# Optimization experiments

Measured on AMD Instinct MI355X. Metric: run time of the kernel, lower is better.

The kernel has to match this reference:

```python
import jax, jax.numpy as jnp
import numpy as np

EPS = 1e-05  # epsilon for Cholesky regularization


def setup_inputs() -> dict:
    key = jax.random.key(0)
    k1, k2, k3 = jax.random.split(key, 3)
    B, H, W, C, I = 32, 64, 64, 64, 4
    x = jax.random.normal(k1, (B, H, W, C, I), dtype=jnp.float32)
    # affine params: identity-like weight plus noise, small bias
    eye = jnp.eye(I, dtype=jnp.float32)[..., None]  # (I, I, 1)
    weight = jnp.broadcast_to(eye, (I, I, C)) + 0.05 * jax.random.normal(k2, (I, I, C), dtype=jnp.float32)
    bias = 0.05 * jax.random.normal(k3, (I, C), dtype=jnp.float32)
    return {"x": x, "weight": weight, "bias": bias}


def reference(x, weight, bias):
    # x: (B, H, W, C, I); training-mode batch stats
    B, H, W, C, I = x.shape
    n = B * H * W
    mean = jnp.mean(x, axis=(0, 1, 2))                       # (C, I)
    xc = x - mean                                            # centered, (B,H,W,C,I)
    cov = jnp.einsum('bhwci,bhwcj->cij', xc, xc) / n         # per-channel (I, I) covariance
    cov = cov + EPS * jnp.eye(I, dtype=x.dtype)
    L = jnp.linalg.cholesky(cov)                             # (C, I, I), lower
    eye = jnp.broadcast_to(jnp.eye(I, dtype=x.dtype), (C, I, I))
    Linv = jax.lax.linalg.triangular_solve(L, eye, left_side=True, lower=True)  # (C, I, I)
    x_norm = jnp.einsum('cij,bhwcj->bhwci', Linv, xc)        # whitened
    # affine: out_i = sum_j weight[i, j, c] * x_norm[..., c, j] + bias[i, c]
    out = jnp.einsum('ijc,bhwcj->bhwci', weight, x_norm) + bias.T
    return out
```

## Files before the change

### kernel.cpp

```cpp
#include <hip/hip_runtime.h>
#include <math.h>

#define EPSREG 1e-5f

typedef float vf4 __attribute__((ext_vector_type(4)));

__global__ __launch_bounds__(256) void stats_kernel(const vf4* __restrict__ x,
                                                    float* __restrict__ stats,
                                                    int pos_per_slice) {
    int tid  = threadIdx.x;
    int c    = tid & 63;
    int lane = tid >> 6;
    int s    = blockIdx.x * 4 + lane;

    const vf4* xp = x + (size_t)s * pos_per_slice * 64 + c;

    float a0=0.f,a1=0.f,a2=0.f,a3=0.f;
    float p00=0.f,p01=0.f,p02=0.f,p03=0.f;
    float p11=0.f,p12=0.f,p13=0.f;
    float p22=0.f,p23=0.f,p33=0.f;

    for (int it = 0; it < pos_per_slice; it += 8) {
        vf4 v[8];
        #pragma unroll
        for (int u = 0; u < 8; ++u) v[u] = xp[(it + u) * 64];
        #pragma unroll
        for (int u = 0; u < 8; ++u) {
            float x0 = v[u].x, x1 = v[u].y, x2 = v[u].z, x3 = v[u].w;
            a0 += x0; a1 += x1; a2 += x2; a3 += x3;
            p00 += x0*x0; p01 += x0*x1; p02 += x0*x2; p03 += x0*x3;
            p11 += x1*x1; p12 += x1*x2; p13 += x1*x3;
            p22 += x2*x2; p23 += x2*x3;
            p33 += x3*x3;
        }
    }

    __shared__ float sm[14 * 256];
    float vals[14] = {a0,a1,a2,a3,p00,p01,p02,p03,p11,p12,p13,p22,p23,p33};
    #pragma unroll
    for (int k = 0; k < 14; ++k) sm[k * 256 + tid] = vals[k];
    __syncthreads();

    if (tid < 64) {
        #pragma unroll
        for (int k = 0; k < 14; ++k) {
            float v = sm[k*256 + tid] + sm[k*256 + 64 + tid]
                    + sm[k*256 + 128 + tid] + sm[k*256 + 192 + tid];
            atomicAdd(&stats[k * 64 + tid], v);
        }
    }
}

__global__ void solve_kernel(const float* __restrict__ stats,
                             const float* __restrict__ weight,
                             const float* __restrict__ bias,
                             float* __restrict__ params,
                             float inv_n) {
    int c = threadIdx.x;
    if (c >= 64) return;

    float m0 = stats[0*64+c]*inv_n, m1 = stats[1*64+c]*inv_n;
    float m2 = stats[2*64+c]*inv_n, m3 = stats[3*64+c]*inv_n;
    float c00 = stats[4*64+c]*inv_n  - m0*m0 + EPSREG;
    float c01 = stats[5*64+c]*inv_n  - m0*m1;
    float c02 = stats[6*64+c]*inv_n  - m0*m2;
    float c03 = stats[7*64+c]*inv_n  - m0*m3;
    float c11 = stats[8*64+c]*inv_n  - m1*m1 + EPSREG;
    float c12 = stats[9*64+c]*inv_n  - m1*m2;
    float c13 = stats[10*64+c]*inv_n - m1*m3;
    float c22 = stats[11*64+c]*inv_n - m2*m2 + EPSREG;
    float c23 = stats[12*64+c]*inv_n - m2*m3;
    float c33 = stats[13*64+c]*inv_n - m3*m3 + EPSREG;

    float l00 = sqrtf(c00);
    float l10 = c01 / l00, l20 = c02 / l00, l30 = c03 / l00;
    float l11 = sqrtf(c11 - l10*l10);
    float l21 = (c12 - l20*l10) / l11;
    float l31 = (c13 - l30*l10) / l11;
    float l22 = sqrtf(c22 - l20*l20 - l21*l21);
    float l32 = (c23 - l30*l20 - l31*l21) / l22;
    float l33 = sqrtf(c33 - l30*l30 - l31*l31 - l32*l32);

    float i00 = 1.f / l00, i11 = 1.f / l11, i22 = 1.f / l22, i33 = 1.f / l33;
    float i10 = -i11 * (l10 * i00);
    float i20 = -i22 * (l20 * i00 + l21 * i10);
    float i21 = -i22 * (l21 * i11);
    float i30 = -i33 * (l30 * i00 + l31 * i10 + l32 * i20);
    float i31 = -i33 * (l31 * i11 + l32 * i21);
    float i32 = -i33 * (l32 * i22);

    float Li[4][4] = {{i00, 0.f, 0.f, 0.f},
                      {i10, i11, 0.f, 0.f},
                      {i20, i21, i22, 0.f},
                      {i30, i31, i32, i33}};

    float* pp = params + c * 25;
    #pragma unroll
    for (int i = 0; i < 4; ++i) {
        float w0 = weight[(i*4 + 0)*64 + c];
        float w1 = weight[(i*4 + 1)*64 + c];
        float w2 = weight[(i*4 + 2)*64 + c];
        float w3 = weight[(i*4 + 3)*64 + c];
        #pragma unroll
        for (int j = 0; j < 4; ++j) {
            pp[i*4 + j] = w0*Li[0][j] + w1*Li[1][j] + w2*Li[2][j] + w3*Li[3][j];
        }
    }
    pp[16] = m0; pp[17] = m1; pp[18] = m2; pp[19] = m3;
    pp[20] = bias[0*64 + c];
    pp[21] = bias[1*64 + c];
    pp[22] = bias[2*64 + c];
    pp[23] = bias[3*64 + c];
    pp[24] = 0.f;
}

__global__ __launch_bounds__(256) void apply_kernel(const vf4* __restrict__ x,
                                                    vf4* __restrict__ out,
                                                    const float* __restrict__ params,
                                                    int total4) {
    int tid0   = blockIdx.x * blockDim.x + threadIdx.x;
    int stride = gridDim.x * blockDim.x;
    int c      = tid0 & 63;

    const float* pp = params + c * 25;
    float M[16];
    #pragma unroll
    for (int k = 0; k < 16; ++k) M[k] = pp[k];
    float m0 = pp[16], m1 = pp[17], m2 = pp[18], m3 = pp[19];
    float b0 = pp[20], b1 = pp[21], b2 = pp[22], b3 = pp[23];

    int i = tid0;
    for (; i + 3 * stride < total4; i += 4 * stride) {
        vf4 v[4];
        #pragma unroll
        for (int u = 0; u < 4; ++u) v[u] = x[i + u * stride];
        #pragma unroll
        for (int u = 0; u < 4; ++u) {
            float x0 = v[u].x - m0, x1 = v[u].y - m1, x2 = v[u].z - m2, x3 = v[u].w - m3;
            vf4 o;
            o.x = M[0]*x0  + M[1]*x1  + M[2]*x2  + M[3]*x3  + b0;
            o.y = M[4]*x0  + M[5]*x1  + M[6]*x2  + M[7]*x3  + b1;
            o.z = M[8]*x0  + M[9]*x1  + M[10]*x2 + M[11]*x3 + b2;
            o.w = M[12]*x0 + M[13]*x1 + M[14]*x2 + M[15]*x3 + b3;
            __builtin_nontemporal_store(o, &out[i + u * stride]);
        }
    }
    for (; i < total4; i += stride) {
        vf4 v = x[i];
        float x0 = v.x - m0, x1 = v.y - m1, x2 = v.z - m2, x3 = v.w - m3;
        vf4 o;
        o.x = M[0]*x0  + M[1]*x1  + M[2]*x2  + M[3]*x3  + b0;
        o.y = M[4]*x0  + M[5]*x1  + M[6]*x2  + M[7]*x3  + b1;
        o.z = M[8]*x0  + M[9]*x1  + M[10]*x2 + M[11]*x3 + b2;
        o.w = M[12]*x0 + M[13]*x1 + M[14]*x2 + M[15]*x3 + b3;
        __builtin_nontemporal_store(o, &out[i]);
    }
}

extern "C" void kernel_launch(void* const* d_in, const int* in_sizes, int n_in,
                              void* d_out, int out_size, void* d_ws, size_t ws_size,
                              hipStream_t stream) {
    const float* x      = (const float*)d_in[0];
    const float* weight = (const float*)d_in[1];
    const float* bias   = (const float*)d_in[2];
    float* out = (float*)d_out;

    float* stats  = (float*)d_ws;
    float* params = (float*)((char*)d_ws + 4096);

    int n_elem = in_sizes[0];
    int npos   = n_elem / 256;
    int total4 = n_elem / 4;

    (void)hipMemsetAsync(stats, 0, 14 * 64 * sizeof(float), stream);

    int pos_per_slice = npos / 2048;
    stats_kernel<<<512, 256, 0, stream>>>((const vf4*)x, stats, pos_per_slice);
    solve_kernel<<<1, 64, 0, stream>>>(stats, weight, bias, params, 1.0f / (float)npos);
    apply_kernel<<<2048, 256, 0, stream>>>((const vf4*)x, (vf4*)out, params, total4);
}
```

Baseline: 265.2 us.

## Fuse stats, solve and apply into one persistent kernel with grid barrier

Merges the three kernels into one 512-block kernel. Each block accumulates partial moments, atomically adds them, then waits on a global counter barrier. After the barrier every thread recomputes its channel's Cholesky/whitening matrix in registers and re-reads its own slice of x to write the output. This removes two launches and the params round-trip, and can let the second read of x hit in cache (x is 64 MiB, so reuse depends on the last-level cache). It relies on all 512 blocks being co-resident, otherwise the spin barrier deadlocks, and every thread now repeats the small solve.

```diff
diff --git a/kernel.cpp b/kernel.cpp
--- a/kernel.cpp
+++ b/kernel.cpp
@@ -2,25 +2,31 @@
 #include <math.h>
 
 #define EPSREG 1e-5f
+#define NBLOCKS 512
 
 typedef float vf4 __attribute__((ext_vector_type(4)));
 
-__global__ __launch_bounds__(256) void stats_kernel(const vf4* __restrict__ x,
+__global__ __launch_bounds__(256) void fused_kernel(const vf4* __restrict__ x,
+                                                    const float* __restrict__ weight,
+                                                    const float* __restrict__ bias,
+                                                    vf4* __restrict__ out,
                                                     float* __restrict__ stats,
-                                                    int pos_per_slice) {
+                                                    unsigned int* __restrict__ counter,
+                                                    int pps,
+                                                    float inv_n) {
     int tid  = threadIdx.x;
     int c    = tid & 63;
     int lane = tid >> 6;
     int s    = blockIdx.x * 4 + lane;
 
-    const vf4* xp = x + (size_t)s * pos_per_slice * 64 + c;
+    const vf4* xp = x + (size_t)s * pps * 64 + c;
 
     float a0=0.f,a1=0.f,a2=0.f,a3=0.f;
     float p00=0.f,p01=0.f,p02=0.f,p03=0.f;
     float p11=0.f,p12=0.f,p13=0.f;
     float p22=0.f,p23=0.f,p33=0.f;
 
-    for (int it = 0; it < pos_per_slice; it += 8) {
+    for (int it = 0; it < pps; it += 8) {
         vf4 v[8];
         #pragma unroll
         for (int u = 0; u < 8; ++u) v[u] = xp[(it + u) * 64];
@@ -36,9 +42,11 @@
     }
 
     __shared__ float sm[14 * 256];
-    float vals[14] = {a0,a1,a2,a3,p00,p01,p02,p03,p11,p12,p13,p22,p23,p33};
-    #pragma unroll
-    for (int k = 0; k < 14; ++k) sm[k * 256 + tid] = vals[k];
+    {
+        float vals[14] = {a0,a1,a2,a3,p00,p01,p02,p03,p11,p12,p13,p22,p23,p33};
+        #pragma unroll
+        for (int k = 0; k < 14; ++k) sm[k * 256 + tid] = vals[k];
+    }
     __syncthreads();
 
     if (tid < 64) {
@@ -49,28 +57,34 @@
             atomicAdd(&stats[k * 64 + tid], v);
         }
     }
-}
+    __syncthreads();
 
-__global__ void solve_kernel(const float* __restrict__ stats,
-                             const float* __restrict__ weight,
-                             const float* __restrict__ bias,
-                             float* __restrict__ params,
-                             float inv_n) {
-    int c = threadIdx.x;
-    if (c >= 64) return;
+    if (tid == 0) {
+        __threadfence();
+        __hip_atomic_fetch_add(counter, 1u, __ATOMIC_ACQ_REL, __HIP_MEMORY_SCOPE_AGENT);
+        while (__hip_atomic_load(counter, __ATOMIC_ACQUIRE, __HIP_MEMORY_SCOPE_AGENT)
+               < (unsigned int)NBLOCKS) {
+            __builtin_amdgcn_s_sleep(8);
+        }
+    }
+    __syncthreads();
 
-    float m0 = stats[0*64+c]*inv_n, m1 = stats[1*64+c]*inv_n;
-    float m2 = stats[2*64+c]*inv_n, m3 = stats[3*64+c]*inv_n;
-    float c00 = stats[4*64+c]*inv_n  - m0*m0 + EPSREG;
-    float c01 = stats[5*64+c]*inv_n  - m0*m1;
-    float c02 = stats[6*64+c]*inv_n  - m0*m2;
-    float c03 = stats[7*64+c]*inv_n  - m0*m3;
-    float c11 = stats[8*64+c]*inv_n  - m1*m1 + EPSREG;
-    float c12 = stats[9*64+c]*inv_n  - m1*m2;
-    float c13 = stats[10*64+c]*inv_n - m1*m3;
-    float c22 = stats[11*64+c]*inv_n - m2*m2 + EPSREG;
-    float c23 = stats[12*64+c]*inv_n - m2*m3;
-    float c33 = stats[13*64+c]*inv_n - m3*m3 + EPSREG;
+    float st[14];
+    #pragma unroll
+    for (int k = 0; k < 14; ++k)
+        st[k] = __hip_atomic_load(&stats[k*64 + c], __ATOMIC_RELAXED, __HIP_MEMORY_SCOPE_AGENT);
+
+    float m0 = st[0]*inv_n, m1 = st[1]*inv_n, m2 = st[2]*inv_n, m3 = st[3]*inv_n;
+    float c00 = st[4]*inv_n  - m0*m0 + EPSREG;
+    float c01 = st[5]*inv_n  - m0*m1;
+    float c02 = st[6]*inv_n  - m0*m2;
+    float c03 = st[7]*inv_n  - m0*m3;
+    float c11 = st[8]*inv_n  - m1*m1 + EPSREG;
+    float c12 = st[9]*inv_n  - m1*m2;
+    float c13 = st[10]*inv_n - m1*m3;
+    float c22 = st[11]*inv_n - m2*m2 + EPSREG;
+    float c23 = st[12]*inv_n - m2*m3;
+    float c33 = st[13]*inv_n - m3*m3 + EPSREG;
 
     float l00 = sqrtf(c00);
     float l10 = c01 / l00, l20 = c02 / l00, l30 = c03 / l00;
@@ -94,7 +108,7 @@
                       {i20, i21, i22, 0.f},
                       {i30, i31, i32, i33}};
 
-    float* pp = params + c * 25;
+    float M[16], b[4];
     #pragma unroll
     for (int i = 0; i < 4; ++i) {
         float w0 = weight[(i*4 + 0)*64 + c];
@@ -102,58 +116,28 @@
         float w2 = weight[(i*4 + 2)*64 + c];
         float w3 = weight[(i*4 + 3)*64 + c];
         #pragma unroll
-        for (int j = 0; j < 4; ++j) {
-            pp[i*4 + j] = w0*Li[0][j] + w1*Li[1][j] + w2*Li[2][j] + w3*Li[3][j];
-        }
+        for (int j = 0; j < 4; ++j)
+            M[i*4 + j] = w0*Li[0][j] + w1*Li[1][j] + w2*Li[2][j] + w3*Li[3][j];
+        b[i] = bias[i*64 + c];
     }
-    pp[16] = m0; pp[17] = m1; pp[18] = m2; pp[19] = m3;
-    pp[20] = bias[0*64 + c];
-    pp[21] = bias[1*64 + c];
-    pp[22] = bias[2*64 + c];
-    pp[23] = bias[3*64 + c];
-    pp[24] = 0.f;
-}
 
-__global__ __launch_bounds__(256) void apply_kernel(const vf4* __restrict__ x,
-                                                    vf4* __restrict__ out,
-                                                    const float* __restrict__ params,
-                                                    int total4) {
-    int tid0   = blockIdx.x * blockDim.x + threadIdx.x;
-    int stride = gridDim.x * blockDim.x;
-    int c      = tid0 & 63;
+    const vf4* xc = x   + (size_t)blockIdx.x * 4 * pps * 64;
+    vf4*       oc = out + (size_t)blockIdx.x * 4 * pps * 64;
 
-    const float* pp = params + c * 25;
-    float M[16];
-    #pragma unroll
-    for (int k = 0; k < 16; ++k) M[k] = pp[k];
-    float m0 = pp[16], m1 = pp[17], m2 = pp[18], m3 = pp[19];
-    float b0 = pp[20], b1 = pp[21], b2 = pp[22], b3 = pp[23];
-
-    int i = tid0;
-    for (; i + 3 * stride < total4; i += 4 * stride) {
+    for (int it = 0; it < pps; it += 4) {
         vf4 v[4];
         #pragma unroll
-        for (int u = 0; u < 4; ++u) v[u] = x[i + u * stride];
+        for (int u = 0; u < 4; ++u) v[u] = xc[(it + u) * 256 + tid];
         #pragma unroll
         for (int u = 0; u < 4; ++u) {
             float x0 = v[u].x - m0, x1 = v[u].y - m1, x2 = v[u].z - m2, x3 = v[u].w - m3;
             vf4 o;
-            o.x = M[0]*x0  + M[1]*x1  + M[2]*x2  + M[3]*x3  + b0;
-            o.y = M[4]*x0  + M[5]*x1  + M[6]*x2  + M[7]*x3  + b1;
-            o.z = M[8]*x0  + M[9]*x1  + M[10]*x2 + M[11]*x3 + b2;
-            o.w = M[12]*x0 + M[13]*x1 + M[14]*x2 + M[15]*x3 + b3;
-            __builtin_nontemporal_store(o, &out[i + u * stride]);
+            o.x = M[0]*x0  + M[1]*x1  + M[2]*x2  + M[3]*x3  + b[0];
+            o.y = M[4]*x0  + M[5]*x1  + M[6]*x2  + M[7]*x3  + b[1];
+            o.z = M[8]*x0  + M[9]*x1  + M[10]*x2 + M[11]*x3 + b[2];
+            o.w = M[12]*x0 + M[13]*x1 + M[14]*x2 + M[15]*x3 + b[3];
+            __builtin_nontemporal_store(o, &oc[(it + u) * 256 + tid]);
         }
-    }
-    for (; i < total4; i += stride) {
-        vf4 v = x[i];
-        float x0 = v.x - m0, x1 = v.y - m1, x2 = v.z - m2, x3 = v.w - m3;
-        vf4 o;
-        o.x = M[0]*x0  + M[1]*x1  + M[2]*x2  + M[3]*x3  + b0;
-        o.y = M[4]*x0  + M[5]*x1  + M[6]*x2  + M[7]*x3  + b1;
-        o.z = M[8]*x0  + M[9]*x1  + M[10]*x2 + M[11]*x3 + b2;
-        o.w = M[12]*x0 + M[13]*x1 + M[14]*x2 + M[15]*x3 + b3;
-        __builtin_nontemporal_store(o, &out[i]);
     }
 }
 
@@ -163,19 +147,18 @@
     const float* x      = (const float*)d_in[0];
     const float* weight = (const float*)d_in[1];
     const float* bias   = (const float*)d_in[2];
-    float* out = (float*)d_out;
+    vf4* out = (vf4*)d_out;
 
-    float* stats  = (float*)d_ws;
-    float* params = (float*)((char*)d_ws + 4096);
+    float*        stats   = (float*)d_ws;
+    unsigned int* counter = (unsigned int*)((char*)d_ws + 4096);
 
     int n_elem = in_sizes[0];
     int npos   = n_elem / 256;
-    int total4 = n_elem / 4;
+    int pps    = npos / (NBLOCKS * 4);
 
-    (void)hipMemsetAsync(stats, 0, 14 * 64 * sizeof(float), stream);
+    (void)hipMemsetAsync(d_ws, 0, 8192, stream);
 
-    int pos_per_slice = npos / 2048;
-    stats_kernel<<<512, 256, 0, stream>>>((const vf4*)x, stats, pos_per_slice);
-    solve_kernel<<<1, 64, 0, stream>>>(stats, weight, bias, params, 1.0f / (float)npos);
-    apply_kernel<<<2048, 256, 0, stream>>>((const vf4*)x, (vf4*)out, params, total4);
+    fused_kernel<<<NBLOCKS, 256, 0, stream>>>((const vf4*)x, weight, bias, out,
+                                              stats, counter, pps,
+                                              1.0f / (float)npos);
 }
```

Result: slower. 311.3 us (+17.4%).
